# Kernel optimization log

Hardware: AMD Instinct MI355X
Metric: run time of the kernel (lower is better)

## Reference

```python
import jax, jax.numpy as jnp
import numpy as np

LEAK = 0.01
EPS = 1e-5


def _gcn(x, W, b, src, dst, n):
    # GCNConv: add self-loops, symmetric D^-1/2 (A+I) D^-1/2 normalization
    h = x @ W
    loop = jnp.arange(n)
    s = jnp.concatenate([src, loop])
    d = jnp.concatenate([dst, loop])
    deg = jax.ops.segment_sum(jnp.ones(s.shape[0], h.dtype), d, num_segments=n)
    dinv = jnp.where(deg > 0, jax.lax.rsqrt(deg), 0.0)
    norm = dinv[s] * dinv[d]
    out = jax.ops.segment_sum(h[s] * norm[:, None], d, num_segments=n)
    return out + b


def _sage(x, Wl, bl, Wr, src, dst, n):
    # SAGEConv (mean aggr): lin_l(mean_neigh) + lin_r(x); bias on lin_l
    cnt = jax.ops.segment_sum(jnp.ones(src.shape[0], x.dtype), dst, num_segments=n)
    agg = jax.ops.segment_sum(x[src], dst, num_segments=n) / jnp.maximum(cnt, 1.0)[:, None]
    return agg @ Wl + bl + x @ Wr


def _bn(x, g, b):
    # BatchNorm over node dim, batch statistics (training forward), biased var
    m = x.mean(0)
    v = jnp.mean((x - m) ** 2, axis=0)
    return (x - m) * jax.lax.rsqrt(v + EPS) * g + b


def _lrelu(x):
    return jnp.where(x >= 0, x, LEAK * x)


def setup_inputs() -> dict:
    key = jax.random.key(0)
    ks = jax.random.split(key, 20)
    N, E, F_IN, H, G, L = 50000, 800000, 128, 128, 1000, 1000
    h2, h4, OUT = H // 2, H // 4, 32
    x = jax.random.normal(ks[0], (N, F_IN), dtype=jnp.float32)
    edge_index = jax.random.randint(ks[1], (2, E), 0, N)
    batch = jnp.sort(jax.random.randint(ks[2], (N,), 0, G))
    link_indices = jax.random.randint(ks[3], (2, L), 0, G)
    s = 0.05
    return {
        "x": x, "edge_index": edge_index, "batch": batch,
        "link_indices": link_indices, "num_graphs": G,
        "W1": jax.random.normal(ks[4], (F_IN, H), jnp.float32) * s,
        "b1": jnp.zeros((H,), jnp.float32),
        "g1": jnp.ones((H,), jnp.float32), "be1": jnp.zeros((H,), jnp.float32),
        "Wl2": jax.random.normal(ks[5], (H, h2), jnp.float32) * s,
        "bl2": jnp.zeros((h2,), jnp.float32),
        "Wr2": jax.random.normal(ks[6], (H, h2), jnp.float32) * s,
        "g2": jnp.ones((h2,), jnp.float32), "be2": jnp.zeros((h2,), jnp.float32),
        "W3": jax.random.normal(ks[7], (h2, h4), jnp.float32) * s,
        "b3": jnp.zeros((h4,), jnp.float32),
        "g3": jnp.ones((h4,), jnp.float32), "be3": jnp.zeros((h4,), jnp.float32),
        "W4": jax.random.normal(ks[8], (h4, OUT), jnp.float32) * s,
        "b4": jnp.zeros((OUT,), jnp.float32),
    }


def reference(x, edge_index, batch, link_indices, num_graphs,
              W1, b1, g1, be1, Wl2, bl2, Wr2, g2, be2,
              W3, b3, g3, be3, W4, b4):
    n = x.shape[0]
    src, dst = edge_index[0], edge_index[1]
    h = _lrelu(_bn(_gcn(x, W1, b1, src, dst, n), g1, be1))        # dropout = identity (eval)
    h = _lrelu(_bn(_sage(h, Wl2, bl2, Wr2, src, dst, n), g2, be2))
    h = _lrelu(_bn(_gcn(h, W3, b3, src, dst, n), g3, be3))
    h = _gcn(h, W4, b4, src, dst, n)
    g = jax.ops.segment_sum(h, batch, num_segments=num_graphs)     # global_add_pool
    src_emb = g[link_indices[0]]
    tgt_emb = g[link_indices[1]]
    return jax.nn.sigmoid(jnp.sum(src_emb * tgt_emb, axis=1))
```

## Files before the change

kernel.cpp:

```cpp
#include <hip/hip_runtime.h>
#include <math.h>

#define LEAK 0.01f
#define BNEPS 1e-5f
#define NCH 256
#define NGMAX 1024

typedef __attribute__((ext_vector_type(8))) short bf16x8;
typedef __attribute__((ext_vector_type(4))) float f32x4;
typedef __attribute__((ext_vector_type(2))) float f32x2;

__device__ inline unsigned bfpack(float a, float b) {
  unsigned ua = __float_as_uint(a);
  unsigned ub = __float_as_uint(b);
  unsigned ra = (ua + 0x7fffu + ((ua >> 16) & 1u)) >> 16;
  unsigned rb = (ub + 0x7fffu + ((ub >> 16) & 1u)) & 0xffff0000u;
  return ra | rb;
}
__device__ inline unsigned short bfround(float a) {
  unsigned ua = __float_as_uint(a);
  return (unsigned short)((ua + 0x7fffu + ((ua >> 16) & 1u)) >> 16);
}
__device__ inline float2 bfunpack(unsigned u) {
  float2 r;
  r.x = __uint_as_float(u << 16);
  r.y = __uint_as_float(u & 0xffff0000u);
  return r;
}
__device__ inline unsigned char f32_to_fp8(float v) {
  int p = __builtin_amdgcn_cvt_pk_fp8_f32(v, v, 0, false);
  return (unsigned char)(p & 0xff);
}

__global__ __launch_bounds__(256) void k_hist(const int* __restrict__ dst,
                                              int* __restrict__ H, int E, int NBK) {
  __shared__ int h[256];
  h[threadIdx.x] = 0;
  __syncthreads();
  int chunk = (E + NCH - 1) / NCH;
  int lo = blockIdx.x * chunk, hi = min(lo + chunk, E);
  for (int e = lo + threadIdx.x; e < hi; e += 256)
    atomicAdd(&h[dst[e] >> 8], 1);
  __syncthreads();
  if (threadIdx.x < NBK) H[threadIdx.x * NCH + blockIdx.x] = h[threadIdx.x];
}

__global__ __launch_bounds__(256) void k_gscan1(const int* __restrict__ in,
                                                int* __restrict__ bsum, int m) {
  int i = blockIdx.x * 256 + threadIdx.x;
  int v = (i < m) ? in[i] : 0;
#pragma unroll
  for (int s = 1; s < 64; s <<= 1) v += __shfl_xor(v, s, 64);
  __shared__ int ws[4];
  if ((threadIdx.x & 63) == 0) ws[threadIdx.x >> 6] = v;
  __syncthreads();
  if (threadIdx.x == 0) bsum[blockIdx.x] = ws[0] + ws[1] + ws[2] + ws[3];
}
__global__ __launch_bounds__(256) void k_gscan2(int* __restrict__ bsum, int NB) {
  __shared__ int lds[256];
  int t = threadIdx.x;
  int v = (t < NB) ? bsum[t] : 0;
  lds[t] = v;
  __syncthreads();
  for (int ofs = 1; ofs < 256; ofs <<= 1) {
    int u = (t >= ofs) ? lds[t - ofs] : 0;
    __syncthreads();
    lds[t] += u;
    __syncthreads();
  }
  if (t < NB) bsum[t] = lds[t] - v;
}
__global__ __launch_bounds__(256) void k_gscan3(const int* __restrict__ in,
                                                const int* __restrict__ boff,
                                                int* __restrict__ out, int m) {
  __shared__ int lds[256];
  int t = threadIdx.x;
  int i = blockIdx.x * 256 + t;
  int v = (i < m) ? in[i] : 0;
  lds[t] = v;
  __syncthreads();
  for (int ofs = 1; ofs < 256; ofs <<= 1) {
    int u = (t >= ofs) ? lds[t - ofs] : 0;
    __syncthreads();
    lds[t] += u;
    __syncthreads();
  }
  if (i < m) out[i] = boff[blockIdx.x] + lds[t] - v;
}

__global__ __launch_bounds__(256) void k_scatter_bkt(
    const int* __restrict__ src, const int* __restrict__ dst,
    const int* __restrict__ O, int* __restrict__ ebuf, int E, int NBK) {
  __shared__ int cur[256];
  if (threadIdx.x < NBK) cur[threadIdx.x] = O[threadIdx.x * NCH + blockIdx.x];
  __syncthreads();
  int chunk = (E + NCH - 1) / NCH;
  int lo = blockIdx.x * chunk, hi = min(lo + chunk, E);
  for (int e = lo + threadIdx.x; e < hi; e += 256) {
    int d = dst[e];
    int pos = atomicAdd(&cur[d >> 8], 1);
    ebuf[pos] = src[e] | ((d & 255) << 24);
  }
}

__global__ __launch_bounds__(256) void k_fill2(
    const int* __restrict__ ebuf, const int* __restrict__ O,
    int* __restrict__ eidx, int* __restrict__ rowptr,
    float* __restrict__ dinv, float* __restrict__ invcnt,
    int E, int n, int NBK) {
  __shared__ int hist[256];
  __shared__ int sc[256];
  __shared__ int cur[256];
  const int b = blockIdx.x;
  const int t = threadIdx.x;
  const int lo = O[b * NCH];
  const int hi = (b + 1 < NBK) ? O[(b + 1) * NCH] : E;
  hist[t] = 0;
  __syncthreads();
  for (int e = lo + t; e < hi; e += 256)
    atomicAdd(&hist[(ebuf[e] >> 24) & 255], 1);
  __syncthreads();
  int v = hist[t];
  sc[t] = v;
  __syncthreads();
  for (int ofs = 1; ofs < 256; ofs <<= 1) {
    int u = (t >= ofs) ? sc[t - ofs] : 0;
    __syncthreads();
    sc[t] += u;
    __syncthreads();
  }
  int excl = sc[t] - v;
  cur[t] = lo + excl;
  int node = b * 256 + t;
  if (node < n) {
    rowptr[node] = lo + excl;
    float d = (float)v;
    dinv[node]   = rsqrtf(d + 1.0f);
    invcnt[node] = 1.0f / fmaxf(d, 1.0f);
  }
  if (node == n || (b == NBK - 1 && t == 255)) rowptr[n] = E;
  __syncthreads();
  for (int e = lo + t; e < hi; e += 256) {
    int p = ebuf[e];
    int pos = atomicAdd(&cur[(p >> 24) & 255], 1);
    eidx[pos] = p & 0xFFFFFF;
  }
}

template<int F, bool GCN, bool OUTBF, bool ADD>
__global__ __launch_bounds__(256) void k_gather(
    const unsigned short* __restrict__ Hs, const float* __restrict__ scale,
    const int* __restrict__ rowptr, const int* __restrict__ eidx,
    const float* __restrict__ bias, const float* __restrict__ addf,
    float* __restrict__ outf, unsigned short* __restrict__ outb, int n) {
  constexpr int COLS = F / 8;
  constexpr int EPI  = 64 / COLS;
  const int v = blockIdx.x * 4 + (threadIdx.x >> 6);
  if (v >= n) return;
  const int lane = threadIdx.x & 63;
  const int col  = lane % COLS;
  const int eo   = lane / COLS;

  const int lo = rowptr[v], hi = rowptr[v + 1];
  float a[8] = {0.f,0.f,0.f,0.f,0.f,0.f,0.f,0.f};
  int myE = (lo + lane < hi) ? eidx[lo + lane] : 0;
  for (int base = lo; base < hi; base += 64) {
    int cnt = min(hi - base, 64);
    int nxt = (base + 64 + lane < hi) ? eidx[base + 64 + lane] : 0;
#pragma unroll 4
    for (int t = eo; t < cnt; t += EPI) {
      int s = __shfl(myE, t, 64);
      uint4 hv = *(const uint4*)&Hs[(long long)s * F + col * 8];
      float2 p0 = bfunpack(hv.x), p1 = bfunpack(hv.y);
      float2 p2 = bfunpack(hv.z), p3 = bfunpack(hv.w);
      a[0]+=p0.x; a[1]+=p0.y; a[2]+=p1.x; a[3]+=p1.y;
      a[4]+=p2.x; a[5]+=p2.y; a[6]+=p3.x; a[7]+=p3.y;
    }
    myE = nxt;
  }
#pragma unroll
  for (int m = COLS; m < 64; m <<= 1) {
#pragma unroll
    for (int j = 0; j < 8; j++) a[j] += __shfl_xor(a[j], m, 64);
  }
  if (eo == 0) {
    float sv = scale[v];
    float o[8];
    if constexpr (GCN) {
      uint4 hv = *(const uint4*)&Hs[(long long)v * F + col * 8];
      float2 p0 = bfunpack(hv.x), p1 = bfunpack(hv.y);
      float2 p2 = bfunpack(hv.z), p3 = bfunpack(hv.w);
      float h[8] = {p0.x,p0.y,p1.x,p1.y,p2.x,p2.y,p3.x,p3.y};
#pragma unroll
      for (int j = 0; j < 8; j++) o[j] = bias[col * 8 + j] + sv * (a[j] + h[j]);
    } else if constexpr (ADD) {
      const float4 t0 = *(const float4*)&addf[(long long)v * F + col * 8];
      const float4 t1 = *(const float4*)&addf[(long long)v * F + col * 8 + 4];
      o[0]=fmaf(sv,a[0],t0.x); o[1]=fmaf(sv,a[1],t0.y);
      o[2]=fmaf(sv,a[2],t0.z); o[3]=fmaf(sv,a[3],t0.w);
      o[4]=fmaf(sv,a[4],t1.x); o[5]=fmaf(sv,a[5],t1.y);
      o[6]=fmaf(sv,a[6],t1.z); o[7]=fmaf(sv,a[7],t1.w);
    } else {
#pragma unroll
      for (int j = 0; j < 8; j++) o[j] = sv * a[j];
    }
    if constexpr (OUTBF) {
      uint4 u;
      u.x = bfpack(o[0], o[1]); u.y = bfpack(o[2], o[3]);
      u.z = bfpack(o[4], o[5]); u.w = bfpack(o[6], o[7]);
      *(uint4*)&outb[(long long)v * F + col * 8] = u;
    } else {
      float4 o0 = {o[0],o[1],o[2],o[3]}, o1 = {o[4],o[5],o[6],o[7]};
      *(float4*)&outf[(long long)v * F + col * 8]     = o0;
      *(float4*)&outf[(long long)v * F + col * 8 + 4] = o1;
    }
  }
}

template<int F, bool GCN, bool ADD>
__global__ __launch_bounds__(256) void k_gather_fp8(
    const unsigned char* __restrict__ Hf8, const unsigned short* __restrict__ Hbf,
    const float* __restrict__ scale,
    const int* __restrict__ rowptr, const int* __restrict__ eidx,
    const float* __restrict__ bias, const float* __restrict__ addf,
    unsigned short* __restrict__ outb, int n) {
  constexpr int COLS = F / 8;
  constexpr int EPI  = 64 / COLS;
  const int v = blockIdx.x * 4 + (threadIdx.x >> 6);
  if (v >= n) return;
  const int lane = threadIdx.x & 63;
  const int col  = lane % COLS;
  const int eo   = lane / COLS;

  const int lo = rowptr[v], hi = rowptr[v + 1];
  float a[8] = {0.f,0.f,0.f,0.f,0.f,0.f,0.f,0.f};
  int myE = (lo + lane < hi) ? eidx[lo + lane] : 0;
  for (int base = lo; base < hi; base += 64) {
    int cnt = min(hi - base, 64);
    int nxt = (base + 64 + lane < hi) ? eidx[base + 64 + lane] : 0;
#pragma unroll 4
    for (int t = eo; t < cnt; t += EPI) {
      int s = __shfl(myE, t, 64);
      uint2 q = *(const uint2*)&Hf8[(long long)s * F + col * 8];
      f32x2 p0 = __builtin_amdgcn_cvt_pk_f32_fp8(q.x, false);
      f32x2 p1 = __builtin_amdgcn_cvt_pk_f32_fp8(q.x, true);
      f32x2 p2 = __builtin_amdgcn_cvt_pk_f32_fp8(q.y, false);
      f32x2 p3 = __builtin_amdgcn_cvt_pk_f32_fp8(q.y, true);
      a[0]+=p0[0]; a[1]+=p0[1]; a[2]+=p1[0]; a[3]+=p1[1];
      a[4]+=p2[0]; a[5]+=p2[1]; a[6]+=p3[0]; a[7]+=p3[1];
    }
    myE = nxt;
  }
#pragma unroll
  for (int m = COLS; m < 64; m <<= 1) {
#pragma unroll
    for (int j = 0; j < 8; j++) a[j] += __shfl_xor(a[j], m, 64);
  }
  if (eo == 0) {
    float sv = scale[v];
    float o[8];
    if constexpr (GCN) {
      uint4 hv = *(const uint4*)&Hbf[(long long)v * F + col * 8];
      float2 p0 = bfunpack(hv.x), p1 = bfunpack(hv.y);
      float2 p2 = bfunpack(hv.z), p3 = bfunpack(hv.w);
      float h[8] = {p0.x,p0.y,p1.x,p1.y,p2.x,p2.y,p3.x,p3.y};
#pragma unroll
      for (int j = 0; j < 8; j++) o[j] = bias[col * 8 + j] + sv * (a[j] + h[j]);
    } else if constexpr (ADD) {
      const float4 t0 = *(const float4*)&addf[(long long)v * F + col * 8];
      const float4 t1 = *(const float4*)&addf[(long long)v * F + col * 8 + 4];
      o[0]=fmaf(sv,a[0],t0.x); o[1]=fmaf(sv,a[1],t0.y);
      o[2]=fmaf(sv,a[2],t0.z); o[3]=fmaf(sv,a[3],t0.w);
      o[4]=fmaf(sv,a[4],t1.x); o[5]=fmaf(sv,a[5],t1.y);
      o[6]=fmaf(sv,a[6],t1.z); o[7]=fmaf(sv,a[7],t1.w);
    } else {
#pragma unroll
      for (int j = 0; j < 8; j++) o[j] = sv * a[j];
    }
    uint4 u;
    u.x = bfpack(o[0], o[1]); u.y = bfpack(o[2], o[3]);
    u.z = bfpack(o[4], o[5]); u.w = bfpack(o[6], o[7]);
    *(uint4*)&outb[(long long)v * F + col * 8] = u;
  }
}

template<int K, int F, bool XBF, bool BNIN, bool F8OUT>
__global__ __launch_bounds__(256) void k_gemm_mfma(
    const void* __restrict__ Xv, const float* __restrict__ W,
    const float* __restrict__ bnstats, const float* __restrict__ prescale,
    unsigned short* __restrict__ Yb, unsigned char* __restrict__ Yf8, int n) {
  constexpr int SP  = K + 8;
  constexpr int NCT = F / 16;
  __shared__ unsigned short sX[64 * SP];
  __shared__ unsigned short sWT[F * SP];
  __shared__ float sbn[BNIN ? 2 * K : 1];

  const int row0 = blockIdx.x * 64;
  if constexpr (BNIN) {
    for (int i = threadIdx.x; i < 2 * K; i += 256) sbn[i] = bnstats[i];
    __syncthreads();
  }
  for (int i = threadIdx.x; i < (K / 2) * F; i += 256) {
    int nn = i % F;
    int kk = (i / F) * 2;
    float w0 = W[(long long)kk * F + nn];
    float w1 = W[(long long)(kk + 1) * F + nn];
    *(unsigned*)&sWT[nn * SP + kk] = bfpack(w0, w1);
  }
  for (int i = threadIdx.x; i < 64 * (K / 8); i += 256) {
    int r = i / (K / 8), k8 = (i % (K / 8)) * 8;
    int gr = row0 + r;
    uint4 u = {0, 0, 0, 0};
    if (gr < n) {
      if constexpr (XBF) {
        const unsigned short* X = (const unsigned short*)Xv;
        uint4 raw = *(const uint4*)&X[(long long)gr * K + k8];
        if constexpr (BNIN) {
          float2 p0 = bfunpack(raw.x), p1 = bfunpack(raw.y);
          float2 p2 = bfunpack(raw.z), p3 = bfunpack(raw.w);
          float y[8] = {p0.x,p0.y,p1.x,p1.y,p2.x,p2.y,p3.x,p3.y};
#pragma unroll
          for (int j = 0; j < 8; j++) {
            float t = fmaf(y[j], sbn[k8 + j], sbn[K + k8 + j]);
            y[j] = (t >= 0.f) ? t : LEAK * t;
          }
          u.x = bfpack(y[0], y[1]); u.y = bfpack(y[2], y[3]);
          u.z = bfpack(y[4], y[5]); u.w = bfpack(y[6], y[7]);
        } else {
          u = raw;
        }
      } else {
        const float* X = (const float*)Xv;
        float4 xa = *(const float4*)&X[(long long)gr * K + k8];
        float4 xb = *(const float4*)&X[(long long)gr * K + k8 + 4];
        u.x = bfpack(xa.x, xa.y); u.y = bfpack(xa.z, xa.w);
        u.z = bfpack(xb.x, xb.y); u.w = bfpack(xb.z, xb.w);
      }
    }
    *(uint4*)&sX[r * SP + k8] = u;
  }
  __syncthreads();

  const int wv   = threadIdx.x >> 6;
  const int lane = threadIdx.x & 63;
  const int l16  = lane & 15;
  const int quad = lane >> 4;
  f32x4 acc[NCT];
#pragma unroll
  for (int c = 0; c < NCT; c++) acc[c] = (f32x4){0.f, 0.f, 0.f, 0.f};

#pragma unroll
  for (int k0 = 0; k0 < K; k0 += 32) {
    bf16x8 af = *(const bf16x8*)&sX[(wv * 16 + l16) * SP + k0 + quad * 8];
#pragma unroll
    for (int c = 0; c < NCT; c++) {
      bf16x8 bfr = *(const bf16x8*)&sWT[(c * 16 + l16) * SP + k0 + quad * 8];
      acc[c] = __builtin_amdgcn_mfma_f32_16x16x32_bf16(af, bfr, acc[c], 0, 0, 0);
    }
  }

  const int rbase = row0 + wv * 16 + quad * 4;
  float ps[4];
#pragma unroll
  for (int rg = 0; rg < 4; rg++) {
    int gr = rbase + rg;
    ps[rg] = (prescale && gr < n) ? prescale[gr] : 1.0f;
  }
#pragma unroll
  for (int c = 0; c < NCT; c++) {
    int col = c * 16 + l16;
#pragma unroll
    for (int rg = 0; rg < 4; rg++) {
      int gr = rbase + rg;
      if (gr < n) {
        float val = acc[c][rg] * ps[rg];
        Yb[(long long)gr * F + col] = bfround(val);
        if constexpr (F8OUT) Yf8[(long long)gr * F + col] = f32_to_fp8(val);
      }
    }
  }
}

__global__ __launch_bounds__(256) void k_gemm_sage_mfma(
    const unsigned short* __restrict__ X, const float* __restrict__ Wl,
    const float* __restrict__ Wr, const float* __restrict__ bl,
    const float* __restrict__ bnstats,
    unsigned char* __restrict__ t1f8, float* __restrict__ t2, int n) {
  constexpr int K = 128, F = 64, SP = K + 8, NCT = F / 16;
  __shared__ unsigned short sX[64 * SP];
  __shared__ unsigned short sWlT[F * SP];
  __shared__ unsigned short sWrT[F * SP];
  __shared__ float sbn[2 * K];

  for (int i = threadIdx.x; i < 2 * K; i += 256) sbn[i] = bnstats[i];
  __syncthreads();
  const int row0 = blockIdx.x * 64;
  for (int i = threadIdx.x; i < (K / 2) * F; i += 256) {
    int nn = i % F;
    int kk = (i / F) * 2;
    *(unsigned*)&sWlT[nn * SP + kk] =
        bfpack(Wl[(long long)kk * F + nn], Wl[(long long)(kk + 1) * F + nn]);
    *(unsigned*)&sWrT[nn * SP + kk] =
        bfpack(Wr[(long long)kk * F + nn], Wr[(long long)(kk + 1) * F + nn]);
  }
  for (int i = threadIdx.x; i < 64 * (K / 8); i += 256) {
    int r = i / (K / 8), k8 = (i % (K / 8)) * 8;
    int gr = row0 + r;
    uint4 u = {0, 0, 0, 0};
    if (gr < n) {
      uint4 raw = *(const uint4*)&X[(long long)gr * K + k8];
      float2 p0 = bfunpack(raw.x), p1 = bfunpack(raw.y);
      float2 p2 = bfunpack(raw.z), p3 = bfunpack(raw.w);
      float y[8] = {p0.x,p0.y,p1.x,p1.y,p2.x,p2.y,p3.x,p3.y};
#pragma unroll
      for (int j = 0; j < 8; j++) {
        float t = fmaf(y[j], sbn[k8 + j], sbn[K + k8 + j]);
        y[j] = (t >= 0.f) ? t : LEAK * t;
      }
      u.x = bfpack(y[0], y[1]); u.y = bfpack(y[2], y[3]);
      u.z = bfpack(y[4], y[5]); u.w = bfpack(y[6], y[7]);
    }
    *(uint4*)&sX[r * SP + k8] = u;
  }
  __syncthreads();

  const int wv   = threadIdx.x >> 6;
  const int lane = threadIdx.x & 63;
  const int l16  = lane & 15;
  const int quad = lane >> 4;
  f32x4 a1[NCT], a2[NCT];
#pragma unroll
  for (int c = 0; c < NCT; c++) {
    a1[c] = (f32x4){0.f, 0.f, 0.f, 0.f};
    a2[c] = (f32x4){0.f, 0.f, 0.f, 0.f};
  }
#pragma unroll
  for (int k0 = 0; k0 < K; k0 += 32) {
    bf16x8 af = *(const bf16x8*)&sX[(wv * 16 + l16) * SP + k0 + quad * 8];
#pragma unroll
    for (int c = 0; c < NCT; c++) {
      bf16x8 bl8 = *(const bf16x8*)&sWlT[(c * 16 + l16) * SP + k0 + quad * 8];
      bf16x8 br8 = *(const bf16x8*)&sWrT[(c * 16 + l16) * SP + k0 + quad * 8];
      a1[c] = __builtin_amdgcn_mfma_f32_16x16x32_bf16(af, bl8, a1[c], 0, 0, 0);
      a2[c] = __builtin_amdgcn_mfma_f32_16x16x32_bf16(af, br8, a2[c], 0, 0, 0);
    }
  }
  const int rbase = row0 + wv * 16 + quad * 4;
#pragma unroll
  for (int c = 0; c < NCT; c++) {
    int col = c * 16 + l16;
    float blv = bl[col];
#pragma unroll
    for (int rg = 0; rg < 4; rg++) {
      int gr = rbase + rg;
      if (gr < n) {
        t1f8[(long long)gr * F + col] = f32_to_fp8(a1[c][rg]);
        t2[(long long)gr * F + col]   = a2[c][rg] + blv;
      }
    }
  }
}

template<int F>
__global__ __launch_bounds__(256) void k_bn_stats(const unsigned short* __restrict__ Y,
                                                  float* __restrict__ partials, int n) {
  constexpr int FP  = F / 2;
  constexpr int RPB = 256 / FP;
  const int f2 = threadIdx.x % FP;
  const int r0 = threadIdx.x / FP;
  const unsigned* Yu = (const unsigned*)Y;
  float s1a = 0.f, s2a = 0.f, s1b = 0.f, s2b = 0.f;
  for (long long r = (long long)blockIdx.x * RPB + r0; r < n; r += 256LL * RPB) {
    float2 p = bfunpack(Yu[r * FP + f2]);
    s1a += p.x; s2a += p.x * p.x;
    s1b += p.y; s2b += p.y * p.y;
  }
  __shared__ float l1a[256], l2a[256], l1b[256], l2b[256];
  l1a[threadIdx.x] = s1a; l2a[threadIdx.x] = s2a;
  l1b[threadIdx.x] = s1b; l2b[threadIdx.x] = s2b;
  __syncthreads();
  if (r0 == 0) {
#pragma unroll
    for (int i = 1; i < RPB; i++) {
      s1a += l1a[i * FP + f2]; s2a += l2a[i * FP + f2];
      s1b += l1b[i * FP + f2]; s2b += l2b[i * FP + f2];
    }
    float* p = &partials[blockIdx.x * 2 * F];
    p[2 * f2]         = s1a;
    p[2 * f2 + 1]     = s1b;
    p[F + 2 * f2]     = s2a;
    p[F + 2 * f2 + 1] = s2b;
  }
}

__global__ void k_bn_finalize(const float* __restrict__ partials, float* __restrict__ stats,
                              const float* __restrict__ g, const float* __restrict__ be,
                              int F, float invN) {
  int f = threadIdx.x;
  if (f >= F) return;
  float s1 = 0.f, s2 = 0.f;
  for (int b = 0; b < 256; b++) {
    s1 += partials[b * 2 * F + f];
    s2 += partials[b * 2 * F + F + f];
  }
  float m   = s1 * invN;
  float var = s2 * invN - m * m;
  float sc  = g[f] * rsqrtf(var + BNEPS);
  stats[f]     = sc;
  stats[F + f] = be[f] - m * sc;
}

__global__ __launch_bounds__(256) void k_pool2(const float* __restrict__ a4,
                                               const int* __restrict__ batch,
                                               float* __restrict__ gpool, int n) {
  int g = blockIdx.x * 4 + (threadIdx.x >> 6);
  if (g >= NGMAX) return;
  int lane = threadIdx.x & 63;
  int s = 0, e = n;
  while (s < e) { int m = (s + e) >> 1; if (batch[m] < g) s = m + 1; else e = m; }
  int s2 = s, e2 = n;
  while (s2 < e2) { int m = (s2 + e2) >> 1; if (batch[m] < g + 1) s2 = m + 1; else e2 = m; }
  int f = lane & 31, ro = lane >> 5;
  float acc = 0.f;
  for (int r = s + ro; r < s2; r += 2) acc += a4[(long long)r * 32 + f];
  acc += __shfl_xor(acc, 32, 64);
  if (lane < 32) gpool[(long long)g * 32 + f] = acc;
}

__global__ void k_link(const float* __restrict__ g, const int* __restrict__ li0,
                       const int* __restrict__ li1, float* __restrict__ out, int L) {
  int i = blockIdx.x * blockDim.x + threadIdx.x;
  if (i >= L) return;
  const float* a = g + (long long)li0[i] * 32;
  const float* b = g + (long long)li1[i] * 32;
  float s = 0.f;
#pragma unroll
  for (int f = 0; f < 32; f++) s = fmaf(a[f], b[f], s);
  out[i] = 1.0f / (1.0f + expf(-s));
}

extern "C" void kernel_launch(void* const* d_in, const int* in_sizes, int n_in,
                              void* d_out, int out_size, void* d_ws, size_t ws_size,
                              hipStream_t stream) {
  const float* x   = (const float*)d_in[0];
  const int* ei    = (const int*)d_in[1];
  const int* batch = (const int*)d_in[2];
  const int* li    = (const int*)d_in[3];
  const float* W1  = (const float*)d_in[5];
  const float* b1  = (const float*)d_in[6];
  const float* g1  = (const float*)d_in[7];
  const float* be1 = (const float*)d_in[8];
  const float* Wl2 = (const float*)d_in[9];
  const float* bl2 = (const float*)d_in[10];
  const float* Wr2 = (const float*)d_in[11];
  const float* g2  = (const float*)d_in[12];
  const float* be2 = (const float*)d_in[13];
  const float* W3  = (const float*)d_in[14];
  const float* b3  = (const float*)d_in[15];
  const float* g3  = (const float*)d_in[16];
  const float* be3 = (const float*)d_in[17];
  const float* W4  = (const float*)d_in[18];
  const float* b4  = (const float*)d_in[19];

  const int n = in_sizes[0] / 128;
  const int E = in_sizes[1] / 2;
  const int L = in_sizes[3] / 2;
  const int* src = ei;
  const int* dst = ei + E;
  const int* li0 = li;
  const int* li1 = li + L;
  const int NBK = (n + 255) / 256;

  char* base = (char*)d_ws;
  size_t off = 0;
  auto alloc = [&](size_t bytes) -> void* {
    void* p = (void*)(base + off);
    off = (off + bytes + 255) & ~(size_t)255;
    return p;
  };
  int*   H      = (int*)alloc((size_t)NBK * NCH * 4);
  int*   O      = (int*)alloc((size_t)NBK * NCH * 4);
  int*   hsum   = (int*)alloc((size_t)1024 * 4);
  int*   ebuf   = (int*)alloc((size_t)E * 4);
  int*   eidx   = (int*)alloc((size_t)E * 4);
  int*   rowptr = (int*)alloc((size_t)(n + 1) * 4);
  float* dinv   = (float*)alloc((size_t)n * 4);
  float* invcnt = (float*)alloc((size_t)n * 4);
  float* stats1 = (float*)alloc(256 * 4);
  float* stats2 = (float*)alloc(128 * 4);
  float* stats3 = (float*)alloc(64 * 4);
  float* partials = (float*)alloc((size_t)256 * 256 * 4);
  float* gpool  = (float*)alloc((size_t)NGMAX * 32 * 4);
  unsigned short* h1b  = (unsigned short*)alloc((size_t)n * 128 * 2);
  unsigned char*  h1f8 = (unsigned char*)alloc((size_t)n * 128);
  unsigned short* a1b  = (unsigned short*)alloc((size_t)n * 128 * 2);
  unsigned char*  t1f8 = (unsigned char*)alloc((size_t)n * 64);
  float*          t2f  = (float*)alloc((size_t)n * 64 * 4);
  unsigned short* h2b  = (unsigned short*)alloc((size_t)n * 64 * 2);
  unsigned short* h3gb = (unsigned short*)alloc((size_t)n * 32 * 2);
  unsigned short* a3b  = (unsigned short*)alloc((size_t)n * 32 * 2);
  unsigned short* h4b  = (unsigned short*)alloc((size_t)n * 32 * 2);
  float*          a4f  = (float*)alloc((size_t)n * 32 * 4);
  (void)ws_size; (void)n_in; (void)out_size;

  const int BT = 256;
  auto cdiv = [](long long a, long long b) { return (int)((a + b - 1) / b); };
  const int GB  = cdiv(n, 4);
  const int GM  = cdiv(n, 64);
  const int MH  = NBK * NCH;
  const int NBH = cdiv(MH, 256);

  k_hist<<<NCH, 256, 0, stream>>>(dst, H, E, NBK);
  k_gscan1<<<NBH, 256, 0, stream>>>(H, hsum, MH);
  k_gscan2<<<1, 256, 0, stream>>>(hsum, NBH);
  k_gscan3<<<NBH, 256, 0, stream>>>(H, hsum, O, MH);
  k_scatter_bkt<<<NCH, 256, 0, stream>>>(src, dst, O, ebuf, E, NBK);
  k_fill2<<<NBK, 256, 0, stream>>>(ebuf, O, eidx, rowptr, dinv, invcnt, E, n, NBK);

  k_gemm_mfma<128,128,false,false,true><<<GM, 256, 0, stream>>>(
      x, W1, nullptr, dinv, h1b, h1f8, n);
  k_gather_fp8<128,true,false><<<GB, 256, 0, stream>>>(
      h1f8, h1b, dinv, rowptr, eidx, b1, nullptr, a1b, n);
  k_bn_stats<128><<<256, 256, 0, stream>>>(a1b, partials, n);
  k_bn_finalize<<<1, 128, 0, stream>>>(partials, stats1, g1, be1, 128, 1.0f / n);

  k_gemm_sage_mfma<<<GM, 256, 0, stream>>>(a1b, Wl2, Wr2, bl2, stats1, t1f8, t2f, n);
  k_gather_fp8<64,false,true><<<GB, 256, 0, stream>>>(
      t1f8, nullptr, invcnt, rowptr, eidx, nullptr, t2f, h2b, n);
  k_bn_stats<64><<<256, 256, 0, stream>>>(h2b, partials, n);
  k_bn_finalize<<<1, 64, 0, stream>>>(partials, stats2, g2, be2, 64, 1.0f / n);

  k_gemm_mfma<64,32,true,true,false><<<GM, 256, 0, stream>>>(
      h2b, W3, stats2, dinv, h3gb, nullptr, n);
  k_gather<32,true,true,false><<<GB, 256, 0, stream>>>(
      h3gb, dinv, rowptr, eidx, b3, nullptr, nullptr, a3b, n);
  k_bn_stats<32><<<256, 256, 0, stream>>>(a3b, partials, n);
  k_bn_finalize<<<1, 32, 0, stream>>>(partials, stats3, g3, be3, 32, 1.0f / n);

  k_gemm_mfma<32,32,true,true,false><<<GM, 256, 0, stream>>>(
      a3b, W4, stats3, dinv, h4b, nullptr, n);
  k_gather<32,true,false,false><<<GB, 256, 0, stream>>>(
      h4b, dinv, rowptr, eidx, b4, nullptr, a4f, nullptr, n);

  k_pool2<<<NGMAX / 4, 256, 0, stream>>>(a4f, batch, gpool, n);
  k_link<<<cdiv(L, BT), BT, 0, stream>>>(gpool, li0, li1, (float*)d_out, L);
}
```

Baseline: 378.8 us.

## Fuse BatchNorm statistics and graph pooling into gather kernels

BN sum and sum-of-squares accumulation moves into the gather epilogue through a shared-memory block reduction plus atomics into 64 slotted partial buffers. BN finalization moves into the following GEMM's prologue, and global add pooling becomes per-node atomics in the last gather. This removes the separate bn_stats, bn_finalize and pool kernels, their extra reads of the activations, and the fp32 a4 buffer. Costs are atomic contention on the slots and pool buffers, and a non-deterministic summation order.

```diff
diff --git a/kernel.cpp b/kernel.cpp
--- a/kernel.cpp
+++ b/kernel.cpp
@@ -5,6 +5,7 @@
 #define BNEPS 1e-5f
 #define NCH 256
 #define NGMAX 1024
+#define NSLOT 64
 
 typedef __attribute__((ext_vector_type(8))) short bf16x8;
 typedef __attribute__((ext_vector_type(4))) float f32x4;
@@ -147,21 +148,26 @@
   }
 }
 
-template<int F, bool GCN, bool OUTBF, bool ADD>
+template<int F, bool FP8, bool GCN, bool ADD, bool STATS, bool POOL>
 __global__ __launch_bounds__(256) void k_gather(
-    const unsigned short* __restrict__ Hs, const float* __restrict__ scale,
+    const void* __restrict__ Hn, const unsigned short* __restrict__ Hbf,
+    const float* __restrict__ scale,
     const int* __restrict__ rowptr, const int* __restrict__ eidx,
     const float* __restrict__ bias, const float* __restrict__ addf,
-    float* __restrict__ outf, unsigned short* __restrict__ outb, int n) {
+    unsigned short* __restrict__ outb,
+    float* __restrict__ partials, const int* __restrict__ batch,
+    float* __restrict__ gpool, int n) {
   constexpr int COLS = F / 8;
   constexpr int EPI  = 64 / COLS;
-  const int v = blockIdx.x * 4 + (threadIdx.x >> 6);
-  if (v >= n) return;
+  const int wid  = threadIdx.x >> 6;
+  const int v    = blockIdx.x * 4 + wid;
+  const bool valid = v < n;
   const int lane = threadIdx.x & 63;
   const int col  = lane % COLS;
   const int eo   = lane / COLS;
 
-  const int lo = rowptr[v], hi = rowptr[v + 1];
+  const int lo = valid ? rowptr[v] : 0;
+  const int hi = valid ? rowptr[v + 1] : 0;
   float a[8] = {0.f,0.f,0.f,0.f,0.f,0.f,0.f,0.f};
   int myE = (lo + lane < hi) ? eidx[lo + lane] : 0;
   for (int base = lo; base < hi; base += 64) {
@@ -170,11 +176,21 @@
 #pragma unroll 4
     for (int t = eo; t < cnt; t += EPI) {
       int s = __shfl(myE, t, 64);
-      uint4 hv = *(const uint4*)&Hs[(long long)s * F + col * 8];
-      float2 p0 = bfunpack(hv.x), p1 = bfunpack(hv.y);
-      float2 p2 = bfunpack(hv.z), p3 = bfunpack(hv.w);
-      a[0]+=p0.x; a[1]+=p0.y; a[2]+=p1.x; a[3]+=p1.y;
-      a[4]+=p2.x; a[5]+=p2.y; a[6]+=p3.x; a[7]+=p3.y;
+      if constexpr (FP8) {
+        uint2 q = *(const uint2*)((const unsigned char*)Hn + (long long)s * F + col * 8);
+        f32x2 p0 = __builtin_amdgcn_cvt_pk_f32_fp8(q.x, false);
+        f32x2 p1 = __builtin_amdgcn_cvt_pk_f32_fp8(q.x, true);
+        f32x2 p2 = __builtin_amdgcn_cvt_pk_f32_fp8(q.y, false);
+        f32x2 p3 = __builtin_amdgcn_cvt_pk_f32_fp8(q.y, true);
+        a[0]+=p0[0]; a[1]+=p0[1]; a[2]+=p1[0]; a[3]+=p1[1];
+        a[4]+=p2[0]; a[5]+=p2[1]; a[6]+=p3[0]; a[7]+=p3[1];
+      } else {
+        uint4 hv = *(const uint4*)((const unsigned short*)Hn + (long long)s * F + col * 8);
+        float2 p0 = bfunpack(hv.x), p1 = bfunpack(hv.y);
+        float2 p2 = bfunpack(hv.z), p3 = bfunpack(hv.w);
+        a[0]+=p0.x; a[1]+=p0.y; a[2]+=p1.x; a[3]+=p1.y;
+        a[4]+=p2.x; a[5]+=p2.y; a[6]+=p3.x; a[7]+=p3.y;
+      }
     }
     myE = nxt;
   }
@@ -183,11 +199,12 @@
 #pragma unroll
     for (int j = 0; j < 8; j++) a[j] += __shfl_xor(a[j], m, 64);
   }
-  if (eo == 0) {
+
+  float o[8] = {0.f,0.f,0.f,0.f,0.f,0.f,0.f,0.f};
+  if (eo == 0 && valid) {
     float sv = scale[v];
-    float o[8];
     if constexpr (GCN) {
-      uint4 hv = *(const uint4*)&Hs[(long long)v * F + col * 8];
+      uint4 hv = *(const uint4*)&Hbf[(long long)v * F + col * 8];
       float2 p0 = bfunpack(hv.x), p1 = bfunpack(hv.y);
       float2 p2 = bfunpack(hv.z), p3 = bfunpack(hv.w);
       float h[8] = {p0.x,p0.y,p1.x,p1.y,p2.x,p2.y,p3.x,p3.y};
@@ -204,100 +221,68 @@
 #pragma unroll
       for (int j = 0; j < 8; j++) o[j] = sv * a[j];
     }
-    if constexpr (OUTBF) {
+    if constexpr (POOL) {
+      int g = batch[v];
+#pragma unroll
+      for (int j = 0; j < 8; j++) atomicAdd(&gpool[(long long)g * F + col * 8 + j], o[j]);
+    } else {
       uint4 u;
       u.x = bfpack(o[0], o[1]); u.y = bfpack(o[2], o[3]);
       u.z = bfpack(o[4], o[5]); u.w = bfpack(o[6], o[7]);
       *(uint4*)&outb[(long long)v * F + col * 8] = u;
-    } else {
-      float4 o0 = {o[0],o[1],o[2],o[3]}, o1 = {o[4],o[5],o[6],o[7]};
-      *(float4*)&outf[(long long)v * F + col * 8]     = o0;
-      *(float4*)&outf[(long long)v * F + col * 8 + 4] = o1;
-    }
-  }
-}
-
-template<int F, bool GCN, bool ADD>
-__global__ __launch_bounds__(256) void k_gather_fp8(
-    const unsigned char* __restrict__ Hf8, const unsigned short* __restrict__ Hbf,
-    const float* __restrict__ scale,
-    const int* __restrict__ rowptr, const int* __restrict__ eidx,
-    const float* __restrict__ bias, const float* __restrict__ addf,
-    unsigned short* __restrict__ outb, int n) {
-  constexpr int COLS = F / 8;
-  constexpr int EPI  = 64 / COLS;
-  const int v = blockIdx.x * 4 + (threadIdx.x >> 6);
-  if (v >= n) return;
-  const int lane = threadIdx.x & 63;
-  const int col  = lane % COLS;
-  const int eo   = lane / COLS;
-
-  const int lo = rowptr[v], hi = rowptr[v + 1];
-  float a[8] = {0.f,0.f,0.f,0.f,0.f,0.f,0.f,0.f};
-  int myE = (lo + lane < hi) ? eidx[lo + lane] : 0;
-  for (int base = lo; base < hi; base += 64) {
-    int cnt = min(hi - base, 64);
-    int nxt = (base + 64 + lane < hi) ? eidx[base + 64 + lane] : 0;
-#pragma unroll 4
-    for (int t = eo; t < cnt; t += EPI) {
-      int s = __shfl(myE, t, 64);
-      uint2 q = *(const uint2*)&Hf8[(long long)s * F + col * 8];
-      f32x2 p0 = __builtin_amdgcn_cvt_pk_f32_fp8(q.x, false);
-      f32x2 p1 = __builtin_amdgcn_cvt_pk_f32_fp8(q.x, true);
-      f32x2 p2 = __builtin_amdgcn_cvt_pk_f32_fp8(q.y, false);
-      f32x2 p3 = __builtin_amdgcn_cvt_pk_f32_fp8(q.y, true);
-      a[0]+=p0[0]; a[1]+=p0[1]; a[2]+=p1[0]; a[3]+=p1[1];
-      a[4]+=p2[0]; a[5]+=p2[1]; a[6]+=p3[0]; a[7]+=p3[1];
-    }
-    myE = nxt;
-  }
-#pragma unroll
-  for (int m = COLS; m < 64; m <<= 1) {
-#pragma unroll
-    for (int j = 0; j < 8; j++) a[j] += __shfl_xor(a[j], m, 64);
-  }
-  if (eo == 0) {
-    float sv = scale[v];
-    float o[8];
-    if constexpr (GCN) {
-      uint4 hv = *(const uint4*)&Hbf[(long long)v * F + col * 8];
-      float2 p0 = bfunpack(hv.x), p1 = bfunpack(hv.y);
-      float2 p2 = bfunpack(hv.z), p3 = bfunpack(hv.w);
-      float h[8] = {p0.x,p0.y,p1.x,p1.y,p2.x,p2.y,p3.x,p3.y};
-#pragma unroll
-      for (int j = 0; j < 8; j++) o[j] = bias[col * 8 + j] + sv * (a[j] + h[j]);
-    } else if constexpr (ADD) {
-      const float4 t0 = *(const float4*)&addf[(long long)v * F + col * 8];
-      const float4 t1 = *(const float4*)&addf[(long long)v * F + col * 8 + 4];
-      o[0]=fmaf(sv,a[0],t0.x); o[1]=fmaf(sv,a[1],t0.y);
-      o[2]=fmaf(sv,a[2],t0.z); o[3]=fmaf(sv,a[3],t0.w);
-      o[4]=fmaf(sv,a[4],t1.x); o[5]=fmaf(sv,a[5],t1.y);
-      o[6]=fmaf(sv,a[6],t1.z); o[7]=fmaf(sv,a[7],t1.w);
-    } else {
-#pragma unroll
-      for (int j = 0; j < 8; j++) o[j] = sv * a[j];
-    }
-    uint4 u;
-    u.x = bfpack(o[0], o[1]); u.y = bfpack(o[2], o[3]);
-    u.z = bfpack(o[4], o[5]); u.w = bfpack(o[6], o[7]);
-    *(uint4*)&outb[(long long)v * F + col * 8] = u;
+    }
+  }
+
+  if constexpr (STATS) {
+    __shared__ float sred[4][2 * F];
+    if (eo == 0) {
+#pragma unroll
+      for (int j = 0; j < 8; j++) {
+        sred[wid][col * 8 + j]     = o[j];
+        sred[wid][F + col * 8 + j] = o[j] * o[j];
+      }
+    }
+    __syncthreads();
+    int t = threadIdx.x;
+    if (t < 2 * F) {
+      float s = sred[0][t] + sred[1][t] + sred[2][t] + sred[3][t];
+      atomicAdd(&partials[(blockIdx.x & (NSLOT - 1)) * 2 * F + t], s);
+    }
   }
 }
 
 template<int K, int F, bool XBF, bool BNIN, bool F8OUT>
 __global__ __launch_bounds__(256) void k_gemm_mfma(
     const void* __restrict__ Xv, const float* __restrict__ W,
-    const float* __restrict__ bnstats, const float* __restrict__ prescale,
-    unsigned short* __restrict__ Yb, unsigned char* __restrict__ Yf8, int n) {
+    const float* __restrict__ pin, const float* __restrict__ gw,
+    const float* __restrict__ bw, float invN,
+    const float* __restrict__ prescale,
+    unsigned short* __restrict__ Yb, unsigned char* __restrict__ Yf8,
+    float* __restrict__ zptr, int zcnt, int n) {
   constexpr int SP  = K + 8;
   constexpr int NCT = F / 16;
   __shared__ unsigned short sX[64 * SP];
   __shared__ unsigned short sWT[F * SP];
   __shared__ float sbn[BNIN ? 2 * K : 1];
 
+  for (int i = blockIdx.x * 256 + threadIdx.x; i < zcnt; i += gridDim.x * 256)
+    zptr[i] = 0.f;
+
   const int row0 = blockIdx.x * 64;
   if constexpr (BNIN) {
-    for (int i = threadIdx.x; i < 2 * K; i += 256) sbn[i] = bnstats[i];
+    int t = threadIdx.x;
+    if (t < K) {
+      float s1 = 0.f, s2 = 0.f;
+      for (int s = 0; s < NSLOT; s++) {
+        s1 += pin[s * 2 * K + t];
+        s2 += pin[s * 2 * K + K + t];
+      }
+      float m   = s1 * invN;
+      float var = s2 * invN - m * m;
+      float scv = gw[t] * rsqrtf(var + BNEPS);
+      sbn[t]     = scv;
+      sbn[K + t] = bw[t] - m * scv;
+    }
     __syncthreads();
   }
   for (int i = threadIdx.x; i < (K / 2) * F; i += 256) {
@@ -384,15 +369,34 @@
 __global__ __launch_bounds__(256) void k_gemm_sage_mfma(
     const unsigned short* __restrict__ X, const float* __restrict__ Wl,
     const float* __restrict__ Wr, const float* __restrict__ bl,
-    const float* __restrict__ bnstats,
-    unsigned char* __restrict__ t1f8, float* __restrict__ t2, int n) {
+    const float* __restrict__ pin, const float* __restrict__ gw,
+    const float* __restrict__ bw, float invN,
+    unsigned char* __restrict__ t1f8, float* __restrict__ t2,
+    float* __restrict__ zptr, int zcnt, int n) {
   constexpr int K = 128, F = 64, SP = K + 8, NCT = F / 16;
   __shared__ unsigned short sX[64 * SP];
   __shared__ unsigned short sWlT[F * SP];
   __shared__ unsigned short sWrT[F * SP];
   __shared__ float sbn[2 * K];
 
-  for (int i = threadIdx.x; i < 2 * K; i += 256) sbn[i] = bnstats[i];
+  for (int i = blockIdx.x * 256 + threadIdx.x; i < zcnt; i += gridDim.x * 256)
+    zptr[i] = 0.f;
+
+  {
+    int t = threadIdx.x;
+    if (t < K) {
+      float s1 = 0.f, s2 = 0.f;
+      for (int s = 0; s < NSLOT; s++) {
+        s1 += pin[s * 2 * K + t];
+        s2 += pin[s * 2 * K + K + t];
+      }
+      float m   = s1 * invN;
+      float var = s2 * invN - m * m;
+      float scv = gw[t] * rsqrtf(var + BNEPS);
+      sbn[t]     = scv;
+      sbn[K + t] = bw[t] - m * scv;
+    }
+  }
   __syncthreads();
   const int row0 = blockIdx.x * 64;
   for (int i = threadIdx.x; i < (K / 2) * F; i += 256) {
@@ -459,72 +463,6 @@
       }
     }
   }
-}
-
-template<int F>
-__global__ __launch_bounds__(256) void k_bn_stats(const unsigned short* __restrict__ Y,
-                                                  float* __restrict__ partials, int n) {
-  constexpr int FP  = F / 2;
-  constexpr int RPB = 256 / FP;
-  const int f2 = threadIdx.x % FP;
-  const int r0 = threadIdx.x / FP;
-  const unsigned* Yu = (const unsigned*)Y;
-  float s1a = 0.f, s2a = 0.f, s1b = 0.f, s2b = 0.f;
-  for (long long r = (long long)blockIdx.x * RPB + r0; r < n; r += 256LL * RPB) {
-    float2 p = bfunpack(Yu[r * FP + f2]);
-    s1a += p.x; s2a += p.x * p.x;
-    s1b += p.y; s2b += p.y * p.y;
-  }
-  __shared__ float l1a[256], l2a[256], l1b[256], l2b[256];
-  l1a[threadIdx.x] = s1a; l2a[threadIdx.x] = s2a;
-  l1b[threadIdx.x] = s1b; l2b[threadIdx.x] = s2b;
-  __syncthreads();
-  if (r0 == 0) {
-#pragma unroll
-    for (int i = 1; i < RPB; i++) {
-      s1a += l1a[i * FP + f2]; s2a += l2a[i * FP + f2];
-      s1b += l1b[i * FP + f2]; s2b += l2b[i * FP + f2];
-    }
-    float* p = &partials[blockIdx.x * 2 * F];
-    p[2 * f2]         = s1a;
-    p[2 * f2 + 1]     = s1b;
-    p[F + 2 * f2]     = s2a;
-    p[F + 2 * f2 + 1] = s2b;
-  }
-}
-
-__global__ void k_bn_finalize(const float* __restrict__ partials, float* __restrict__ stats,
-                              const float* __restrict__ g, const float* __restrict__ be,
-                              int F, float invN) {
-  int f = threadIdx.x;
-  if (f >= F) return;
-  float s1 = 0.f, s2 = 0.f;
-  for (int b = 0; b < 256; b++) {
-    s1 += partials[b * 2 * F + f];
-    s2 += partials[b * 2 * F + F + f];
-  }
-  float m   = s1 * invN;
-  float var = s2 * invN - m * m;
-  float sc  = g[f] * rsqrtf(var + BNEPS);
-  stats[f]     = sc;
-  stats[F + f] = be[f] - m * sc;
-}
-
-__global__ __launch_bounds__(256) void k_pool2(const float* __restrict__ a4,
-                                               const int* __restrict__ batch,
-                                               float* __restrict__ gpool, int n) {
-  int g = blockIdx.x * 4 + (threadIdx.x >> 6);
-  if (g >= NGMAX) return;
-  int lane = threadIdx.x & 63;
-  int s = 0, e = n;
-  while (s < e) { int m = (s + e) >> 1; if (batch[m] < g) s = m + 1; else e = m; }
-  int s2 = s, e2 = n;
-  while (s2 < e2) { int m = (s2 + e2) >> 1; if (batch[m] < g + 1) s2 = m + 1; else e2 = m; }
-  int f = lane & 31, ro = lane >> 5;
-  float acc = 0.f;
-  for (int r = s + ro; r < s2; r += 2) acc += a4[(long long)r * 32 + f];
-  acc += __shfl_xor(acc, 32, 64);
-  if (lane < 32) gpool[(long long)g * 32 + f] = acc;
 }
 
 __global__ void k_link(const float* __restrict__ g, const int* __restrict__ li0,
@@ -586,10 +524,9 @@
   int*   rowptr = (int*)alloc((size_t)(n + 1) * 4);
   float* dinv   = (float*)alloc((size_t)n * 4);
   float* invcnt = (float*)alloc((size_t)n * 4);
-  float* stats1 = (float*)alloc(256 * 4);
-  float* stats2 = (float*)alloc(128 * 4);
-  float* stats3 = (float*)alloc(64 * 4);
-  float* partials = (float*)alloc((size_t)256 * 256 * 4);
+  float* partials1 = (float*)alloc((size_t)NSLOT * 256 * 4);
+  float* partials2 = (float*)alloc((size_t)NSLOT * 128 * 4);
+  float* partials3 = (float*)alloc((size_t)NSLOT * 64 * 4);
   float* gpool  = (float*)alloc((size_t)NGMAX * 32 * 4);
   unsigned short* h1b  = (unsigned short*)alloc((size_t)n * 128 * 2);
   unsigned char*  h1f8 = (unsigned char*)alloc((size_t)n * 128);
@@ -600,7 +537,6 @@
   unsigned short* h3gb = (unsigned short*)alloc((size_t)n * 32 * 2);
   unsigned short* a3b  = (unsigned short*)alloc((size_t)n * 32 * 2);
   unsigned short* h4b  = (unsigned short*)alloc((size_t)n * 32 * 2);
-  float*          a4f  = (float*)alloc((size_t)n * 32 * 4);
   (void)ws_size; (void)n_in; (void)out_size;
 
   const int BT = 256;
@@ -609,6 +545,7 @@
   const int GM  = cdiv(n, 64);
   const int MH  = NBK * NCH;
   const int NBH = cdiv(MH, 256);
+  const float invN = 1.0f / (float)n;
 
   k_hist<<<NCH, 256, 0, stream>>>(dst, H, E, NBK);
   k_gscan1<<<NBH, 256, 0, stream>>>(H, hsum, MH);
@@ -618,30 +555,32 @@
   k_fill2<<<NBK, 256, 0, stream>>>(ebuf, O, eidx, rowptr, dinv, invcnt, E, n, NBK);
 
   k_gemm_mfma<128,128,false,false,true><<<GM, 256, 0, stream>>>(
-      x, W1, nullptr, dinv, h1b, h1f8, n);
-  k_gather_fp8<128,true,false><<<GB, 256, 0, stream>>>(
-      h1f8, h1b, dinv, rowptr, eidx, b1, nullptr, a1b, n);
-  k_bn_stats<128><<<256, 256, 0, stream>>>(a1b, partials, n);
-  k_bn_finalize<<<1, 128, 0, stream>>>(partials, stats1, g1, be1, 128, 1.0f / n);
-
-  k_gemm_sage_mfma<<<GM, 256, 0, stream>>>(a1b, Wl2, Wr2, bl2, stats1, t1f8, t2f, n);
-  k_gather_fp8<64,false,true><<<GB, 256, 0, stream>>>(
-      t1f8, nullptr, invcnt, rowptr, eidx, nullptr, t2f, h2b, n);
-  k_bn_stats<64><<<256, 256, 0, stream>>>(h2b, partials, n);
-  k_bn_finalize<<<1, 64, 0, stream>>>(partials, stats2, g2, be2, 64, 1.0f / n);
+      x, W1, nullptr, nullptr, nullptr, 0.f, dinv, h1b, h1f8,
+      partials1, NSLOT * 256, n);
+  k_gather<128,true,true,false,true,false><<<GB, 256, 0, stream>>>(
+      h1f8, h1b, dinv, rowptr, eidx, b1, nullptr, a1b,
+      partials1, nullptr, nullptr, n);
+
+  k_gemm_sage_mfma<<<GM, 256, 0, stream>>>(
+      a1b, Wl2, Wr2, bl2, partials1, g1, be1, invN, t1f8, t2f,
+      partials2, NSLOT * 128, n);
+  k_gather<64,true,false,true,true,false><<<GB, 256, 0, stream>>>(
+      t1f8, nullptr, invcnt, rowptr, eidx, nullptr, t2f, h2b,
+      partials2, nullptr, nullptr, n);
 
   k_gemm_mfma<64,32,true,true,false><<<GM, 256, 0, stream>>>(
-      h2b, W3, stats2, dinv, h3gb, nullptr, n);
-  k_gather<32,true,true,false><<<GB, 256, 0, stream>>>(
-      h3gb, dinv, rowptr, eidx, b3, nullptr, nullptr, a3b, n);
-  k_bn_stats<32><<<256, 256, 0, stream>>>(a3b, partials, n);
-  k_bn_finalize<<<1, 32, 0, stream>>>(partials, stats3, g3, be3, 32, 1.0f / n);
+      h2b, W3, partials2, g2, be2, invN, dinv, h3gb, nullptr,
+      partials3, NSLOT * 64, n);
+  k_gather<32,false,true,false,true,false><<<GB, 256, 0, stream>>>(
+      h3gb, h3gb, dinv, rowptr, eidx, b3, nullptr, a3b,
+      partials3, nullptr, nullptr, n);
 
   k_gemm_mfma<32,32,true,true,false><<<GM, 256, 0, stream>>>(
-      a3b, W4, stats3, dinv, h4b, nullptr, n);
-  k_gather<32,true,false,false><<<GB, 256, 0, stream>>>(
-      h4b, dinv, rowptr, eidx, b4, nullptr, a4f, nullptr, n);
-
-  k_pool2<<<NGMAX / 4, 256, 0, stream>>>(a4f, batch, gpool, n);
+      a3b, W4, partials3, g3, be3, invN, dinv, h4b, nullptr,
+      gpool, NGMAX * 32, n);
+  k_gather<32,false,true,false,false,true><<<GB, 256, 0, stream>>>(
+      h4b, h4b, dinv, rowptr, eidx, b4, nullptr, nullptr,
+      nullptr, batch, gpool, n);
+
   k_link<<<cdiv(L, BT), BT, 0, stream>>>(gpool, li0, li1, (float*)d_out, L);
 }
```

Measured after the change: 357.6 us. 1.06x faster.
